# Kernel optimization log

Hardware: AMD Instinct MI355X
Metric: run time of the kernel (lower is better)

## Reference

```python
import jax, jax.numpy as jnp
import numpy as np

NUM_ROUTES = 1152
NUM_CAPS = 10
IN_CH = 8
OUT_CH = 16
NUM_ITERS = 3
BATCH = 256


def squash(s, axis=-1, eps=1e-9):
    # standard capsule squash over the capsule-vector (out_channels) axis
    sq_norm = jnp.sum(s * s, axis=axis, keepdims=True)
    return (sq_norm / (1.0 + sq_norm)) * (s / jnp.sqrt(sq_norm + eps))


def setup_inputs() -> dict:
    key = jax.random.key(0)
    kx, kw = jax.random.split(key)
    x = jax.random.normal(kx, (BATCH, NUM_ROUTES, IN_CH), dtype=jnp.float32)
    # kaiming_uniform-ish init: bound = sqrt(6 / fan_in), fan_in = in_channels
    bound = float(np.sqrt(6.0 / IN_CH))
    W = jax.random.uniform(kw, (1, NUM_ROUTES, NUM_CAPS, OUT_CH, IN_CH),
                           dtype=jnp.float32, minval=-bound, maxval=bound)
    return {"x": x, "W": W}


def reference(x, W):
    # x: [B, R, I]; W: [1, R, C, O, I]
    B = x.shape[0]
    Wr = W[0]  # [R, C, O, I]
    # u_hat = W @ x  -> [B, R, C, O] (equivalent to matmul with x unsqueezed)
    u_hat = jnp.einsum('rcoi,bri->brco', Wr, x)

    b_ij = jnp.zeros((NUM_ROUTES, NUM_CAPS), dtype=x.dtype)  # shared over batch
    v_j = None
    c_ij = None
    for it in range(NUM_ITERS):
        c_ij = jax.nn.softmax(b_ij, axis=0)                 # softmax over routes
        s_j = jnp.einsum('rc,brco->bco', c_ij, u_hat)       # [B, C, O]
        v_j = squash(s_j, axis=-1)
        if it < NUM_ITERS - 1:
            # agreement: u_hat^T v, averaged over batch
            a_ij = jnp.einsum('brco,bco->brc', u_hat, v_j)  # [B, R, C]
            b_ij = b_ij + jnp.mean(a_ij, axis=0)

    # match torch output shapes: v_j.squeeze(1) -> [B, C, O, 1]; c_ij -> [B, R, C, 1, 1]
    v_out = v_j[..., None]
    c_out = jnp.broadcast_to(c_ij[None, :, :, None, None],
                             (B, NUM_ROUTES, NUM_CAPS, 1, 1))
    return v_out, c_out
```

## Files before the change

kernel.cpp:

```cpp
#include <hip/hip_runtime.h>
#include <math.h>


typedef __attribute__((ext_vector_type(8))) short short8v;
typedef __attribute__((ext_vector_type(4))) float f32x4;

__device__ __forceinline__ unsigned short f2bf(float f) {
    unsigned u = __float_as_uint(f);
    u += 0x7FFFu + ((u >> 16) & 1u);
    return (unsigned short)(u >> 16);
}
__device__ __forceinline__ float bf2f(unsigned short h) {
    return __uint_as_float(((unsigned)h) << 16);
}

__global__ __launch_bounds__(256) void k_prep(const float* __restrict__ x,
                                              const float* __restrict__ W,
                                              unsigned short* __restrict__ xh,
                                              unsigned short* __restrict__ xl,
                                              unsigned short* __restrict__ wph,
                                              unsigned short* __restrict__ wpl,
                                              unsigned short* __restrict__ xTh,
                                              unsigned short* __restrict__ xTl)
{
    const int tid = threadIdx.x;
    if (blockIdx.x < 2304) {
        const int i = blockIdx.x * 256 + tid;
        const float4 v = reinterpret_cast<const float4*>(x)[i];
        const unsigned short h0 = f2bf(v.x), h1 = f2bf(v.y), h2 = f2bf(v.z), h3 = f2bf(v.w);
        const unsigned short l0 = f2bf(v.x - bf2f(h0)), l1 = f2bf(v.y - bf2f(h1)),
                             l2 = f2bf(v.z - bf2f(h2)), l3 = f2bf(v.w - bf2f(h3));
        reinterpret_cast<uint2*>(xh)[i] =
            make_uint2((unsigned)h0 | ((unsigned)h1 << 16), (unsigned)h2 | ((unsigned)h3 << 16));
        reinterpret_cast<uint2*>(xl)[i] =
            make_uint2((unsigned)l0 | ((unsigned)l1 << 16), (unsigned)l2 | ((unsigned)l3 << 16));
    } else if (blockIdx.x < 2880) {
        __shared__ float raw[2560];
        const int r0 = (blockIdx.x - 2304) * 2;
        const float sc = 1.0f / 1152.0f;
        const float4* __restrict__ W4 = reinterpret_cast<const float4*>(W) + (size_t)r0 * 320;
#pragma unroll
        for (int q = 0; q < 3; ++q) {
            const int idx = q * 256 + tid;
            if (idx < 640) *reinterpret_cast<float4*>(&raw[idx * 4]) = W4[idx];
        }
        __syncthreads();
#pragma unroll
        for (int q = 0; q < 10; ++q) {
            const int idx = q * 256 + tid;
            const int n = idx >> 4, kloc = idx & 15;
            const int rl = kloc >> 3, i = kloc & 7, c = n >> 4, o = n & 15;
            const float wv = raw[rl * 1280 + c * 128 + o * 8 + i] * sc;
            const unsigned short h = f2bf(wv);
            const size_t off = (size_t)n * 9216 + r0 * 8 + kloc;
            wph[off] = h;
            wpl[off] = f2bf(wv - bf2f(h));
        }
    } else {
        __shared__ short Th[16][256];
        __shared__ short Tl[16][256];
        const int m0 = (blockIdx.x - 2880) * 16;
        const int b = tid;
#pragma unroll
        for (int q = 0; q < 4; ++q) {
            const float4 v = reinterpret_cast<const float4*>(x)[(size_t)b * 2304 + (m0 >> 2) + q];
            const unsigned short h0 = f2bf(v.x), h1 = f2bf(v.y), h2 = f2bf(v.z), h3 = f2bf(v.w);
            Th[q * 4 + 0][b] = (short)h0;
            Th[q * 4 + 1][b] = (short)h1;
            Th[q * 4 + 2][b] = (short)h2;
            Th[q * 4 + 3][b] = (short)h3;
            Tl[q * 4 + 0][b] = (short)f2bf(v.x - bf2f(h0));
            Tl[q * 4 + 1][b] = (short)f2bf(v.y - bf2f(h1));
            Tl[q * 4 + 2][b] = (short)f2bf(v.z - bf2f(h2));
            Tl[q * 4 + 3][b] = (short)f2bf(v.w - bf2f(h3));
        }
        __syncthreads();
        const int m = tid >> 4, seg = tid & 15;
        const size_t o = (size_t)(m0 + m) * 256 + seg * 16;
        *reinterpret_cast<uint4*>(xTh + o) = *reinterpret_cast<const uint4*>(&Th[m][seg * 16]);
        *reinterpret_cast<uint4*>(xTh + o + 8) = *reinterpret_cast<const uint4*>(&Th[m][seg * 16 + 8]);
        *reinterpret_cast<uint4*>(xTl + o) = *reinterpret_cast<const uint4*>(&Tl[m][seg * 16]);
        *reinterpret_cast<uint4*>(xTl + o + 8) = *reinterpret_cast<const uint4*>(&Tl[m][seg * 16 + 8]);
    }
}

__global__ __launch_bounds__(256) void k_scale2(const float* __restrict__ W,
                                                const float* __restrict__ cw,
                                                unsigned short* __restrict__ wph,
                                                unsigned short* __restrict__ wpl)
{
    __shared__ float raw[2560];
    __shared__ float cl[20];
    const int r0 = blockIdx.x * 2;
    const int tid = threadIdx.x;
    if (tid < 20) cl[tid] = cw[r0 * 10 + tid];
    const float4* __restrict__ W4 = reinterpret_cast<const float4*>(W) + (size_t)r0 * 320;
#pragma unroll
    for (int q = 0; q < 3; ++q) {
        const int idx = q * 256 + tid;
        if (idx < 640) *reinterpret_cast<float4*>(&raw[idx * 4]) = W4[idx];
    }
    __syncthreads();
#pragma unroll
    for (int q = 0; q < 10; ++q) {
        const int idx = q * 256 + tid;
        const int n = idx >> 4, kloc = idx & 15;
        const int rl = kloc >> 3, i = kloc & 7, c = n >> 4, o = n & 15;
        const float wv = raw[rl * 1280 + c * 128 + o * 8 + i] * cl[rl * 10 + c];
        const unsigned short h = f2bf(wv);
        const size_t off = (size_t)n * 9216 + r0 * 8 + kloc;
        wph[off] = h;
        wpl[off] = f2bf(wv - bf2f(h));
    }
}

__global__ __launch_bounds__(256) void k_sM(const unsigned short* __restrict__ xh,
                                            const unsigned short* __restrict__ xl,
                                            const unsigned short* __restrict__ wph,
                                            const unsigned short* __restrict__ wpl,
                                            float* __restrict__ s_part)
{
    __shared__ alignas(16) short Bs[2][12][80][8];
    const int bid = blockIdx.x;
    const int kb = bid >> 3;
    const int mt = (bid >> 1) & 3;
    const int nt = bid & 1;
    const int tid  = threadIdx.x;
    const int w    = tid >> 6;
    const int lane = tid & 63;
    const int l15  = lane & 15;
    const int lqw  = lane >> 4;
    const int row  = mt * 64 + w * 16 + l15;
    const int n0   = nt * 80;

    short8v ah[3], al[3];
    const size_t arow = (size_t)row * 9216 + kb * 96 + lqw * 8;
#pragma unroll
    for (int ks = 0; ks < 3; ++ks) {
        ah[ks] = *reinterpret_cast<const short8v*>(xh + arow + ks * 32);
        al[ks] = *reinterpret_cast<const short8v*>(xl + arow + ks * 32);
    }

    for (int idx = tid; idx < 960; idx += 256) {
        const int n = idx / 12, ch = idx % 12;
        const size_t g = (size_t)(n0 + n) * 9216 + kb * 96 + ch * 8;
        *reinterpret_cast<short8v*>(&Bs[0][ch][n][0]) =
            *reinterpret_cast<const short8v*>(wph + g);
        *reinterpret_cast<short8v*>(&Bs[1][ch][n][0]) =
            *reinterpret_cast<const short8v*>(wpl + g);
    }
    __syncthreads();

    f32x4 acc[5];
#pragma unroll
    for (int t = 0; t < 5; ++t) acc[t] = (f32x4){0.f, 0.f, 0.f, 0.f};

#pragma unroll
    for (int ks = 0; ks < 3; ++ks) {
        const int ch = ks * 4 + lqw;
#pragma unroll
        for (int t = 0; t < 5; ++t) {
            const short8v bh = *reinterpret_cast<const short8v*>(&Bs[0][ch][t * 16 + l15][0]);
            const short8v bl = *reinterpret_cast<const short8v*>(&Bs[1][ch][t * 16 + l15][0]);
            acc[t] = __builtin_amdgcn_mfma_f32_16x16x32_bf16(ah[ks], bh, acc[t], 0, 0, 0);
            acc[t] = __builtin_amdgcn_mfma_f32_16x16x32_bf16(ah[ks], bl, acc[t], 0, 0, 0);
            acc[t] = __builtin_amdgcn_mfma_f32_16x16x32_bf16(al[ks], bh, acc[t], 0, 0, 0);
        }
    }

    const int crow0 = mt * 64 + w * 16 + lqw * 4;
#pragma unroll
    for (int t = 0; t < 5; ++t) {
#pragma unroll
        for (int v = 0; v < 4; ++v) {
            s_part[((size_t)kb * 256 + crow0 + v) * 160 + n0 + t * 16 + l15] = acc[t][v];
        }
    }
}

__global__ __launch_bounds__(192) void k_rvT(const float* __restrict__ s_part,
                                             unsigned short* __restrict__ vTh,
                                             unsigned short* __restrict__ vTl)
{
    const int b = blockIdx.x;
    const int n = threadIdx.x;
    if (n < 160) {
        const float* p = s_part + (size_t)b * 160 + n;
        float s0 = 0.f, s1 = 0.f, s2 = 0.f, s3 = 0.f, s4 = 0.f, s5 = 0.f, s6 = 0.f, s7 = 0.f;
#pragma unroll
        for (int kbv = 0; kbv < 96; kbv += 8) {
            s0 += p[(size_t)(kbv + 0) * 40960];
            s1 += p[(size_t)(kbv + 1) * 40960];
            s2 += p[(size_t)(kbv + 2) * 40960];
            s3 += p[(size_t)(kbv + 3) * 40960];
            s4 += p[(size_t)(kbv + 4) * 40960];
            s5 += p[(size_t)(kbv + 5) * 40960];
            s6 += p[(size_t)(kbv + 6) * 40960];
            s7 += p[(size_t)(kbv + 7) * 40960];
        }
        const float s = ((s0 + s1) + (s2 + s3)) + ((s4 + s5) + (s6 + s7));
        float sq = s * s;
#pragma unroll
        for (int off = 1; off < 16; off <<= 1) sq += __shfl_xor(sq, off, 16);
        const float scale = (sq / (1.f + sq)) / sqrtf(sq + 1e-9f);
        const float val = s * scale;
        const unsigned short h = f2bf(val);
        vTh[n * 256 + b] = h;
        vTl[n * 256 + b] = f2bf(val - bf2f(h));
    }
}

__global__ __launch_bounds__(128) void k_aM(const unsigned short* __restrict__ vTh,
                                            const unsigned short* __restrict__ vTl,
                                            const unsigned short* __restrict__ xTh,
                                            const unsigned short* __restrict__ xTl,
                                            const float* __restrict__ W,
                                            float* __restrict__ dbp)
{
    __shared__ float dbl[20];
    const int mt = blockIdx.x >> 1;
    const int kh = blockIdx.x & 1;
    const int m0 = mt * 16;
    const int r0 = m0 >> 3;
    const int b0 = kh * 128;
    const int tid  = threadIdx.x;
    const int w    = tid >> 6;
    const int lane = tid & 63;
    const int l15  = lane & 15;
    const int lqw  = lane >> 4;
    if (tid < 20) dbl[tid] = 0.f;

    const size_t xbase = (size_t)(m0 + l15) * 256 + b0 + lqw * 8;

    f32x4 acc[5];
#pragma unroll
    for (int t = 0; t < 5; ++t) acc[t] = (f32x4){0.f, 0.f, 0.f, 0.f};

#pragma unroll
    for (int ks = 0; ks < 4; ++ks) {
        const short8v bh = *reinterpret_cast<const short8v*>(xTh + xbase + ks * 32);
        const short8v bl = *reinterpret_cast<const short8v*>(xTl + xbase + ks * 32);
#pragma unroll
        for (int t = 0; t < 5; ++t) {
            const size_t vbase = (size_t)(w * 80 + t * 16 + l15) * 256 + b0 + lqw * 8 + ks * 32;
            const short8v ah = *reinterpret_cast<const short8v*>(vTh + vbase);
            const short8v al = *reinterpret_cast<const short8v*>(vTl + vbase);
            acc[t] = __builtin_amdgcn_mfma_f32_16x16x32_bf16(ah, bh, acc[t], 0, 0, 0);
            acc[t] = __builtin_amdgcn_mfma_f32_16x16x32_bf16(ah, bl, acc[t], 0, 0, 0);
            acc[t] = __builtin_amdgcn_mfma_f32_16x16x32_bf16(al, bh, acc[t], 0, 0, 0);
        }
    }

    __syncthreads();
    const int rloc = l15 >> 3;
    const int i = l15 & 7;
    const int r = r0 + rloc;
#pragma unroll
    for (int t = 0; t < 5; ++t) {
        const int c = w * 5 + t;
        const float* wp = &W[(((size_t)(r * 10 + c) * 16 + lqw * 4) * 8) + i];
        float pv = wp[0] * acc[t][0] + wp[8] * acc[t][1] + wp[16] * acc[t][2] + wp[24] * acc[t][3];
        pv += __shfl_xor(pv, 16);
        pv += __shfl_xor(pv, 32);
        pv += __shfl_xor(pv, 1);
        pv += __shfl_xor(pv, 2);
        pv += __shfl_xor(pv, 4);
        if ((lane & 55) == 0)
            dbl[rloc * 10 + c] = pv;
    }
    __syncthreads();
    if (tid < 20) dbp[(size_t)kh * 11520 + (r0 + tid / 10) * 10 + (tid % 10)] = dbl[tid];
}

__global__ __launch_bounds__(128) void k_sm(const float* __restrict__ bprev,
                                            const float* __restrict__ dbp,
                                            float* __restrict__ bnew,
                                            float* __restrict__ cij)
{
    __shared__ float red[2];
    __shared__ float red2[2];
    const int c = blockIdx.x;
    const int tid = threadIdx.x;
    float bv[9];
#pragma unroll
    for (int j = 0; j < 9; ++j) {
        const int idx = (tid + j * 128) * 10 + c;
        const float d = dbp[idx] + dbp[11520 + idx];
        bv[j] = (bprev ? bprev[idx] : 0.f) + d * (1.0f / 256.0f);
    }
    float mx = bv[0];
#pragma unroll
    for (int j = 1; j < 9; ++j) mx = fmaxf(mx, bv[j]);
#pragma unroll
    for (int off = 1; off < 64; off <<= 1) mx = fmaxf(mx, __shfl_xor(mx, off, 64));
    if ((tid & 63) == 0) red[tid >> 6] = mx;
    __syncthreads();
    mx = fmaxf(red[0], red[1]);
    float es[9], lsum = 0.f;
#pragma unroll
    for (int j = 0; j < 9; ++j) { es[j] = expf(bv[j] - mx); lsum += es[j]; }
#pragma unroll
    for (int off = 1; off < 64; off <<= 1) lsum += __shfl_xor(lsum, off, 64);
    if ((tid & 63) == 0) red2[tid >> 6] = lsum;
    __syncthreads();
    const float inv = 1.f / (red2[0] + red2[1]);
#pragma unroll
    for (int j = 0; j < 9; ++j) {
        const int idx = (tid + j * 128) * 10 + c;
        bnew[idx] = bv[j];
        cij[idx] = es[j] * inv;
    }
}

__global__ __launch_bounds__(256) void k_rvc(const float* __restrict__ s_part,
                                             const float* __restrict__ cij,
                                             float* __restrict__ out)
{
    const int tid = threadIdx.x;
    if (blockIdx.x < 160) {
        const int e = blockIdx.x * 256 + tid;
        float s0 = 0.f, s1 = 0.f, s2 = 0.f, s3 = 0.f;
#pragma unroll
        for (int kbv = 0; kbv < 96; kbv += 4) {
            s0 += s_part[(size_t)(kbv + 0) * 40960 + e];
            s1 += s_part[(size_t)(kbv + 1) * 40960 + e];
            s2 += s_part[(size_t)(kbv + 2) * 40960 + e];
            s3 += s_part[(size_t)(kbv + 3) * 40960 + e];
        }
        const float s = (s0 + s1) + (s2 + s3);
        float sq = s * s;
#pragma unroll
        for (int off = 1; off < 16; off <<= 1) sq += __shfl_xor(sq, off, 16);
        const float scale = (sq / (1.f + sq)) / sqrtf(sq + 1e-9f);
        out[e] = s * scale;
    } else {
        const int i = (blockIdx.x - 160) * 256 + tid;
        const float4 v = reinterpret_cast<const float4*>(cij)[i % 2880];
        reinterpret_cast<float4*>(out + 40960)[i] = v;
    }
}

extern "C" void kernel_launch(void* const* d_in, const int* in_sizes, int n_in,
                              void* d_out, int out_size, void* d_ws, size_t ws_size,
                              hipStream_t stream)
{
    const float* x = (const float*)d_in[0];
    const float* W = (const float*)d_in[1];
    float* out = (float*)d_out;

    unsigned short* xh  = (unsigned short*)d_ws;
    unsigned short* xl  = xh + 2359296;
    unsigned short* xTh = xl + 2359296;
    unsigned short* xTl = xTh + 2359296;
    unsigned short* wph = xTl + 2359296;
    unsigned short* wpl = wph + 1474560;
    unsigned short* vTh = wpl + 1474560;
    unsigned short* vTl = vTh + 40960;
    float* s_part = (float*)(vTl + 40960 + 32);
    float* b1   = s_part + 3932160;
    float* b2   = b1 + 11520;
    float* c2   = b2 + 11520;
    float* c3   = c2 + 11520;
    float* dbp0 = c3 + 11520;
    float* dbp1 = dbp0 + 23040;

    k_prep<<<3456, 256, 0, stream>>>(x, W, xh, xl, wph, wpl, xTh, xTl);

    k_sM<<<768, 256, 0, stream>>>(xh, xl, wph, wpl, s_part);
    k_rvT<<<256, 192, 0, stream>>>(s_part, vTh, vTl);
    k_aM<<<1152, 128, 0, stream>>>(vTh, vTl, xTh, xTl, W, dbp0);
    k_sm<<<10, 128, 0, stream>>>(nullptr, dbp0, b1, c2);

    k_scale2<<<576, 256, 0, stream>>>(W, c2, wph, wpl);
    k_sM<<<768, 256, 0, stream>>>(xh, xl, wph, wpl, s_part);
    k_rvT<<<256, 192, 0, stream>>>(s_part, vTh, vTl);
    k_aM<<<1152, 128, 0, stream>>>(vTh, vTl, xTh, xTl, W, dbp1);
    k_sm<<<10, 128, 0, stream>>>(b1, dbp1, b2, c3);

    k_scale2<<<576, 256, 0, stream>>>(W, c3, wph, wpl);
    k_sM<<<768, 256, 0, stream>>>(xh, xl, wph, wpl, s_part);
    k_rvc<<<3040, 256, 0, stream>>>(s_part, c3, out);
}
```

Measured before the change: 125.8 us.

## Fuse route softmax into W scaling kernel and widen sM tiles to full N

The separate 10-block softmax kernel and the W-scaling kernel become one kernel. Each of its 576 blocks redundantly recomputes the full per-capsule softmax statistics over all 1152 routes, then scales its own slice of W. This removes one launch and a low-parallelism serial stage per iteration, at the cost of every block re-reading the whole dbp/bprev arrays. Separately, k_sM now covers all 160 output columns per block instead of 80. That halves the grid to 384 blocks and the redundant A-fragment loads, but doubles LDS and accumulator registers per block.

Measured after the change: 163.0 us. 1.3x slower.

```diff
diff --git a/kernel.cpp b/kernel.cpp
--- a/kernel.cpp
+++ b/kernel.cpp
@@ -84,54 +84,22 @@
     }
 }
 
-__global__ __launch_bounds__(256) void k_scale2(const float* __restrict__ W,
-                                                const float* __restrict__ cw,
-                                                unsigned short* __restrict__ wph,
-                                                unsigned short* __restrict__ wpl)
-{
-    __shared__ float raw[2560];
-    __shared__ float cl[20];
-    const int r0 = blockIdx.x * 2;
-    const int tid = threadIdx.x;
-    if (tid < 20) cl[tid] = cw[r0 * 10 + tid];
-    const float4* __restrict__ W4 = reinterpret_cast<const float4*>(W) + (size_t)r0 * 320;
-#pragma unroll
-    for (int q = 0; q < 3; ++q) {
-        const int idx = q * 256 + tid;
-        if (idx < 640) *reinterpret_cast<float4*>(&raw[idx * 4]) = W4[idx];
-    }
-    __syncthreads();
-#pragma unroll
-    for (int q = 0; q < 10; ++q) {
-        const int idx = q * 256 + tid;
-        const int n = idx >> 4, kloc = idx & 15;
-        const int rl = kloc >> 3, i = kloc & 7, c = n >> 4, o = n & 15;
-        const float wv = raw[rl * 1280 + c * 128 + o * 8 + i] * cl[rl * 10 + c];
-        const unsigned short h = f2bf(wv);
-        const size_t off = (size_t)n * 9216 + r0 * 8 + kloc;
-        wph[off] = h;
-        wpl[off] = f2bf(wv - bf2f(h));
-    }
-}
-
 __global__ __launch_bounds__(256) void k_sM(const unsigned short* __restrict__ xh,
                                             const unsigned short* __restrict__ xl,
                                             const unsigned short* __restrict__ wph,
                                             const unsigned short* __restrict__ wpl,
                                             float* __restrict__ s_part)
 {
-    __shared__ alignas(16) short Bs[2][12][80][8];
+    __shared__ alignas(16) short Bs[2][12][160][8];
     const int bid = blockIdx.x;
-    const int kb = bid >> 3;
-    const int mt = (bid >> 1) & 3;
-    const int nt = bid & 1;
+    const int kb = bid >> 2;
+    const int mt = bid & 3;
     const int tid  = threadIdx.x;
     const int w    = tid >> 6;
     const int lane = tid & 63;
     const int l15  = lane & 15;
     const int lqw  = lane >> 4;
     const int row  = mt * 64 + w * 16 + l15;
-    const int n0   = nt * 80;
 
     short8v ah[3], al[3];
     const size_t arow = (size_t)row * 9216 + kb * 96 + lqw * 8;
@@ -141,9 +109,9 @@
         al[ks] = *reinterpret_cast<const short8v*>(xl + arow + ks * 32);
     }
 
-    for (int idx = tid; idx < 960; idx += 256) {
+    for (int idx = tid; idx < 1920; idx += 256) {
         const int n = idx / 12, ch = idx % 12;
-        const size_t g = (size_t)(n0 + n) * 9216 + kb * 96 + ch * 8;
+        const size_t g = (size_t)n * 9216 + kb * 96 + ch * 8;
         *reinterpret_cast<short8v*>(&Bs[0][ch][n][0]) =
             *reinterpret_cast<const short8v*>(wph + g);
         *reinterpret_cast<short8v*>(&Bs[1][ch][n][0]) =
@@ -151,15 +119,15 @@
     }
     __syncthreads();
 
-    f32x4 acc[5];
-#pragma unroll
-    for (int t = 0; t < 5; ++t) acc[t] = (f32x4){0.f, 0.f, 0.f, 0.f};
+    f32x4 acc[10];
+#pragma unroll
+    for (int t = 0; t < 10; ++t) acc[t] = (f32x4){0.f, 0.f, 0.f, 0.f};
 
 #pragma unroll
     for (int ks = 0; ks < 3; ++ks) {
         const int ch = ks * 4 + lqw;
 #pragma unroll
-        for (int t = 0; t < 5; ++t) {
+        for (int t = 0; t < 10; ++t) {
             const short8v bh = *reinterpret_cast<const short8v*>(&Bs[0][ch][t * 16 + l15][0]);
             const short8v bl = *reinterpret_cast<const short8v*>(&Bs[1][ch][t * 16 + l15][0]);
             acc[t] = __builtin_amdgcn_mfma_f32_16x16x32_bf16(ah[ks], bh, acc[t], 0, 0, 0);
@@ -170,10 +138,10 @@
 
     const int crow0 = mt * 64 + w * 16 + lqw * 4;
 #pragma unroll
-    for (int t = 0; t < 5; ++t) {
+    for (int t = 0; t < 10; ++t) {
 #pragma unroll
         for (int v = 0; v < 4; ++v) {
-            s_part[((size_t)kb * 256 + crow0 + v) * 160 + n0 + t * 16 + l15] = acc[t][v];
+            s_part[((size_t)kb * 256 + crow0 + v) * 160 + t * 16 + l15] = acc[t][v];
         }
     }
 }
@@ -272,43 +240,103 @@
     if (tid < 20) dbp[(size_t)kh * 11520 + (r0 + tid / 10) * 10 + (tid % 10)] = dbl[tid];
 }
 
-__global__ __launch_bounds__(128) void k_sm(const float* __restrict__ bprev,
-                                            const float* __restrict__ dbp,
-                                            float* __restrict__ bnew,
-                                            float* __restrict__ cij)
-{
-    __shared__ float red[2];
-    __shared__ float red2[2];
-    const int c = blockIdx.x;
+__global__ __launch_bounds__(256) void k_smsc(const float* __restrict__ W,
+                                              const float* __restrict__ bprev,
+                                              const float* __restrict__ dbp,
+                                              float* __restrict__ bnew,
+                                              float* __restrict__ cij,
+                                              unsigned short* __restrict__ wph,
+                                              unsigned short* __restrict__ wpl)
+{
+    __shared__ float raw[2560];
+    __shared__ float wmx[4][10];
+    __shared__ float wsm[4][10];
+    __shared__ float cl[20];
+    const int r0 = blockIdx.x * 2;
     const int tid = threadIdx.x;
-    float bv[9];
-#pragma unroll
-    for (int j = 0; j < 9; ++j) {
-        const int idx = (tid + j * 128) * 10 + c;
-        const float d = dbp[idx] + dbp[11520 + idx];
-        bv[j] = (bprev ? bprev[idx] : 0.f) + d * (1.0f / 256.0f);
-    }
-    float mx = bv[0];
-#pragma unroll
-    for (int j = 1; j < 9; ++j) mx = fmaxf(mx, bv[j]);
-#pragma unroll
-    for (int off = 1; off < 64; off <<= 1) mx = fmaxf(mx, __shfl_xor(mx, off, 64));
-    if ((tid & 63) == 0) red[tid >> 6] = mx;
+    const int lane = tid & 63;
+    const int wv_ = tid >> 6;
+
+    const float4* __restrict__ W4 = reinterpret_cast<const float4*>(W) + (size_t)r0 * 320;
+#pragma unroll
+    for (int q = 0; q < 3; ++q) {
+        const int idx = q * 256 + tid;
+        if (idx < 640) *reinterpret_cast<float4*>(&raw[idx * 4]) = W4[idx];
+    }
+
+    float bv[5][10];
+    float m[10], s[10];
+#pragma unroll
+    for (int c = 0; c < 10; ++c) m[c] = -3.0e38f;
+#pragma unroll
+    for (int j = 0; j < 5; ++j) {
+        const int r = tid + j * 256;
+        if (r < 1152) {
+#pragma unroll
+            for (int c = 0; c < 10; ++c) {
+                const int idx = r * 10 + c;
+                const float v = (bprev ? bprev[idx] : 0.f)
+                              + (dbp[idx] + dbp[11520 + idx]) * (1.0f / 256.0f);
+                bv[j][c] = v;
+                m[c] = fmaxf(m[c], v);
+            }
+        }
+    }
+#pragma unroll
+    for (int c = 0; c < 10; ++c)
+#pragma unroll
+        for (int off = 1; off < 64; off <<= 1) m[c] = fmaxf(m[c], __shfl_xor(m[c], off));
+#pragma unroll
+    for (int c = 0; c < 10; ++c) s[c] = 0.f;
+#pragma unroll
+    for (int j = 0; j < 5; ++j) {
+        const int r = tid + j * 256;
+        if (r < 1152) {
+#pragma unroll
+            for (int c = 0; c < 10; ++c) s[c] += expf(bv[j][c] - m[c]);
+        }
+    }
+#pragma unroll
+    for (int c = 0; c < 10; ++c)
+#pragma unroll
+        for (int off = 1; off < 64; off <<= 1) s[c] += __shfl_xor(s[c], off);
+    if (lane == 0) {
+#pragma unroll
+        for (int c = 0; c < 10; ++c) { wmx[wv_][c] = m[c]; wsm[wv_][c] = s[c]; }
+    }
     __syncthreads();
-    mx = fmaxf(red[0], red[1]);
-    float es[9], lsum = 0.f;
-#pragma unroll
-    for (int j = 0; j < 9; ++j) { es[j] = expf(bv[j] - mx); lsum += es[j]; }
-#pragma unroll
-    for (int off = 1; off < 64; off <<= 1) lsum += __shfl_xor(lsum, off, 64);
-    if ((tid & 63) == 0) red2[tid >> 6] = lsum;
+
+    float M[10], S[10];
+#pragma unroll
+    for (int c = 0; c < 10; ++c) {
+        const float m0_ = fmaxf(fmaxf(wmx[0][c], wmx[1][c]), fmaxf(wmx[2][c], wmx[3][c]));
+        M[c] = m0_;
+        S[c] = wsm[0][c] * expf(wmx[0][c] - m0_) + wsm[1][c] * expf(wmx[1][c] - m0_)
+             + wsm[2][c] * expf(wmx[2][c] - m0_) + wsm[3][c] * expf(wmx[3][c] - m0_);
+    }
+
+    if (tid < 20) {
+        const int rr = r0 + tid / 10, c = tid % 10;
+        const int idx = rr * 10 + c;
+        const float v = (bprev ? bprev[idx] : 0.f)
+                      + (dbp[idx] + dbp[11520 + idx]) * (1.0f / 256.0f);
+        bnew[idx] = v;
+        const float ce = expf(v - M[c]) / S[c];
+        cij[idx] = ce;
+        cl[tid] = ce;
+    }
     __syncthreads();
-    const float inv = 1.f / (red2[0] + red2[1]);
-#pragma unroll
-    for (int j = 0; j < 9; ++j) {
-        const int idx = (tid + j * 128) * 10 + c;
-        bnew[idx] = bv[j];
-        cij[idx] = es[j] * inv;
+
+#pragma unroll
+    for (int q = 0; q < 10; ++q) {
+        const int idx = q * 256 + tid;
+        const int n = idx >> 4, kloc = idx & 15;
+        const int rl = kloc >> 3, i = kloc & 7, c = n >> 4, o = n & 15;
+        const float wvv = raw[rl * 1280 + c * 128 + o * 8 + i] * cl[rl * 10 + c];
+        const unsigned short h = f2bf(wvv);
+        const size_t off = (size_t)n * 9216 + r0 * 8 + kloc;
+        wph[off] = h;
+        wpl[off] = f2bf(wvv - bf2f(h));
     }
 }
 
@@ -366,18 +394,16 @@
 
     k_prep<<<3456, 256, 0, stream>>>(x, W, xh, xl, wph, wpl, xTh, xTl);
 
-    k_sM<<<768, 256, 0, stream>>>(xh, xl, wph, wpl, s_part);
+    k_sM<<<384, 256, 0, stream>>>(xh, xl, wph, wpl, s_part);
     k_rvT<<<256, 192, 0, stream>>>(s_part, vTh, vTl);
     k_aM<<<1152, 128, 0, stream>>>(vTh, vTl, xTh, xTl, W, dbp0);
-    k_sm<<<10, 128, 0, stream>>>(nullptr, dbp0, b1, c2);
-
-    k_scale2<<<576, 256, 0, stream>>>(W, c2, wph, wpl);
-    k_sM<<<768, 256, 0, stream>>>(xh, xl, wph, wpl, s_part);
+    k_smsc<<<576, 256, 0, stream>>>(W, nullptr, dbp0, b1, c2, wph, wpl);
+
+    k_sM<<<384, 256, 0, stream>>>(xh, xl, wph, wpl, s_part);
     k_rvT<<<256, 192, 0, stream>>>(s_part, vTh, vTl);
     k_aM<<<1152, 128, 0, stream>>>(vTh, vTl, xTh, xTl, W, dbp1);
-    k_sm<<<10, 128, 0, stream>>>(b1, dbp1, b2, c3);
-
-    k_scale2<<<576, 256, 0, stream>>>(W, c3, wph, wpl);
-    k_sM<<<768, 256, 0, stream>>>(xh, xl, wph, wpl, s_part);
+    k_smsc<<<576, 256, 0, stream>>>(W, b1, dbp1, b2, c3, wph, wpl);
+
+    k_sM<<<384, 256, 0, stream>>>(xh, xl, wph, wpl, s_part);
     k_rvc<<<3040, 256, 0, stream>>>(s_part, c3, out);
 }
```
